# Kernel optimization log

Measured on AMD Instinct MI355X. Metric: run time of the kernel, lower is better.

Reference implementation:

```python
import jax, jax.numpy as jnp
import numpy as np
from jax import lax

LATENT = 512
HIDDEN = 512
VOCAB = 10
SEQ = 6
BATCH = 32768


def setup_inputs() -> dict:
    key = jax.random.key(0)
    ks = jax.random.split(key, 7)
    s_ih = 1.0 / np.sqrt(HIDDEN)
    return {
        "x": jax.random.normal(ks[0], (BATCH, LATENT), dtype=jnp.float32),
        # PyTorch GRU params, gate order (r, z, n)
        "w_ih": jax.random.uniform(ks[1], (3 * HIDDEN, LATENT), jnp.float32, -s_ih, s_ih),
        "w_hh": jax.random.uniform(ks[2], (3 * HIDDEN, HIDDEN), jnp.float32, -s_ih, s_ih),
        "b_ih": jax.random.uniform(ks[3], (3 * HIDDEN,), jnp.float32, -s_ih, s_ih),
        "b_hh": jax.random.uniform(ks[4], (3 * HIDDEN,), jnp.float32, -s_ih, s_ih),
        "w_out": jax.random.uniform(ks[5], (VOCAB, HIDDEN), jnp.float32, -s_ih, s_ih),
        "b_out": jax.random.uniform(ks[6], (VOCAB,), jnp.float32, -s_ih, s_ih),
    }


def reference(x, w_ih, w_hh, b_ih, b_hh, w_out, b_out):
    # Input to the GRU is x repeated at every timestep, so the input-hidden
    # projection is hoisted out of the time loop (computed once).
    gi = x @ w_ih.T + b_ih                      # (B, 3H), constant over time
    gi_r, gi_z, gi_n = jnp.split(gi, 3, axis=-1)

    def step(h, _):
        gh = h @ w_hh.T + b_hh                  # (B, 3H)
        gh_r, gh_z, gh_n = jnp.split(gh, 3, axis=-1)
        r = jax.nn.sigmoid(gi_r + gh_r)
        z = jax.nn.sigmoid(gi_z + gh_z)
        n = jnp.tanh(gi_n + r * gh_n)
        h_new = (1.0 - z) * n + z * h
        return h_new, h_new

    # Initial hidden state is x itself (hidden_dim == latent_dim).
    _, hs = lax.scan(step, x, None, length=SEQ)  # (SEQ, B, H)
    out = jnp.transpose(hs, (1, 0, 2))           # (B, SEQ, H)
    logits = out @ w_out.T + b_out               # (B, SEQ, VOCAB)
    return logits
```

## Files before the change

kernel.cpp:

```cpp
#include <hip/hip_runtime.h>
#include <hip/hip_bf16.h>
#include <stdint.h>


typedef __bf16 bf16_t;
typedef bf16_t bf16x8 __attribute__((ext_vector_type(8)));
typedef bf16_t bf16x4 __attribute__((ext_vector_type(4)));
typedef float  f32x4  __attribute__((ext_vector_type(4)));
typedef float  f32x2  __attribute__((ext_vector_type(2)));

#define THREADS 512
#define BM      64
#define NBLK    512
#define NSTEP   6

#define WIH_OFF 0u
#define WHH_OFF 1572864u
#define WOP_OFF 3145728u
#define GI_OFF  4194304u
#define HST_OFF 104857600u

static __device__ __forceinline__ float sigm(float v) { return 1.0f / (1.0f + __expf(-v)); }
static __device__ __forceinline__ float tanhf_(float v) {
  v = fminf(fmaxf(v, -12.0f), 12.0f);
  float e = __expf(2.0f * v);
  return 1.0f - 2.0f / (e + 1.0f);
}
static __device__ __forceinline__ f32x4 up4(bf16x4 v) {
  f32x4 o; o[0] = (float)v[0]; o[1] = (float)v[1]; o[2] = (float)v[2]; o[3] = (float)v[3];
  return o;
}
static __device__ __forceinline__ bf16x4 pk4(f32x4 v) {
  bf16x4 o; o[0] = (bf16_t)v[0]; o[1] = (bf16_t)v[1]; o[2] = (bf16_t)v[2]; o[3] = (bf16_t)v[3];
  return o;
}

__global__ void prep_kernel(const float* __restrict__ wih_f, const float* __restrict__ whh_f,
                            const float* __restrict__ wout_f,
                            bf16x8* __restrict__ wihPk, bf16x8* __restrict__ whhPk,
                            bf16x8* __restrict__ wopPk) {
  int c = blockIdx.x * 256 + threadIdx.x;
  int lane = c & 63, l15 = lane & 15, lk = (lane >> 4) & 3;
  if (c < 196608) {
    int cid = (c < 98304) ? c : c - 98304;
    const float* src = (c < 98304) ? wih_f : whh_f;
    bf16x8* dst = (c < 98304) ? wihPk : whhPk;
    int kk = (cid >> 6) & 15;
    int nt = cid >> 10;
    const float* p = src + (size_t)(nt * 16 + l15) * 512 + kk * 32 + lk * 8;
    bf16x8 o;
    #pragma unroll
    for (int i = 0; i < 8; ++i) o[i] = (bf16_t)p[i];
    dst[cid] = o;
  } else if (c < 197632) {
    int cid = c - 196608;
    int kk = cid >> 6;
    bf16x8 o;
    if (l15 < 10) {
      const float* p = wout_f + (size_t)l15 * 512 + kk * 32 + lk * 8;
      #pragma unroll
      for (int i = 0; i < 8; ++i) o[i] = (bf16_t)p[i];
    } else {
      #pragma unroll
      for (int i = 0; i < 8; ++i) o[i] = (bf16_t)0.0f;
    }
    wopPk[cid] = o;
  }
}

__global__ __launch_bounds__(THREADS, 2) void gru_kernel(
    const float* __restrict__ x, const float* __restrict__ b_ih,
    const float* __restrict__ b_hh, const float* __restrict__ b_out,
    const bf16x8* __restrict__ wih, const bf16x8* __restrict__ whh,
    const bf16x8* __restrict__ wop,
    bf16x4* __restrict__ gi, bf16x4* __restrict__ hst, float* __restrict__ out) {
  __shared__ __align__(16) char hlds[BM * 1024];

  const int tid   = (int)threadIdx.x;
  const int lane  = tid & 63;
  const int wq    = tid >> 6;
  const int l15   = lane & 15;
  const int lk    = lane >> 4;
  const int brow0 = (int)blockIdx.x * BM;
  const int swz   = (l15 & 7) << 4;
  const int kbase = (lk * 16) ^ swz;
  const int cbase = (lk * 8) ^ swz;

  #pragma unroll
  for (int it = 0; it < 16; ++it) {
    int f4  = it * THREADS + tid;
    int row = f4 >> 7, c4 = f4 & 127;
    float4 v = ((const float4*)(x + (size_t)(brow0 + row) * 512))[c4];
    bf16x4 h4 = { (bf16_t)v.x, (bf16_t)v.y, (bf16_t)v.z, (bf16_t)v.w };
    *(bf16x4*)(&hlds[row * 1024 + ((c4 * 8) ^ ((row & 7) << 4))]) = h4;
  }
  __syncthreads();

  const size_t gibase = (size_t)blockIdx.x * 24576;
  const size_t hstbase = (size_t)blockIdx.x * 8192;

  #pragma unroll
  for (int p = 0; p < 4; ++p) {
    const int jt = wq * 4 + p;
    f32x4 acc[3][4];
    #pragma unroll
    for (int g = 0; g < 3; ++g)
      #pragma unroll
      for (int bt = 0; bt < 4; ++bt) acc[g][bt] = (f32x4){0.f, 0.f, 0.f, 0.f};

    #pragma unroll 2
    for (int kk = 0; kk < 16; ++kk) {
      bf16x8 hf[4];
      #pragma unroll
      for (int bt = 0; bt < 4; ++bt)
        hf[bt] = *(const bf16x8*)(&hlds[(bt * 16 + l15) * 1024 + ((kk * 64) ^ kbase)]);
      #pragma unroll
      for (int g = 0; g < 3; ++g) {
        bf16x8 wf = wih[((g * 32 + jt) * 16 + kk) * 64 + lane];
        #pragma unroll
        for (int bt = 0; bt < 4; ++bt)
          acc[g][bt] = __builtin_amdgcn_mfma_f32_16x16x32_bf16(wf, hf[bt], acc[g][bt], 0, 0, 0);
      }
    }
    {
      int j = jt * 16 + lk * 4;
      f32x4 b0 = *(const f32x4*)(b_ih + j) + *(const f32x4*)(b_hh + j);
      f32x4 b1 = *(const f32x4*)(b_ih + 512 + j) + *(const f32x4*)(b_hh + 512 + j);
      f32x4 b2 = *(const f32x4*)(b_ih + 1024 + j);
      #pragma unroll
      for (int bt = 0; bt < 4; ++bt) {
        int cb = (jt * 3) * 4 + bt;
        gi[gibase + ((size_t)(cb + 0) << 6) + lane] = pk4(acc[0][bt] + b0);
        gi[gibase + ((size_t)(cb + 4) << 6) + lane] = pk4(acc[1][bt] + b1);
        gi[gibase + ((size_t)(cb + 8) << 6) + lane] = pk4(acc[2][bt] + b2);
      }
    }
  }

  for (int t = 0; t < NSTEP; ++t) {
    #pragma unroll
    for (int p = 0; p < 4; ++p) {
      const int jt = wq * 4 + p;
      const int cb = (jt * 3) * 4;

      f32x4 acc[3][4];
      #pragma unroll
      for (int g = 0; g < 3; ++g)
        #pragma unroll
        for (int bt = 0; bt < 4; ++bt) acc[g][bt] = (f32x4){0.f, 0.f, 0.f, 0.f};

      #pragma unroll 2
      for (int kk = 0; kk < 16; ++kk) {
        bf16x8 hf[4];
        #pragma unroll
        for (int bt = 0; bt < 4; ++bt)
          hf[bt] = *(const bf16x8*)(&hlds[(bt * 16 + l15) * 1024 + ((kk * 64) ^ kbase)]);
        #pragma unroll
        for (int g = 0; g < 3; ++g) {
          bf16x8 wf = whh[((g * 32 + jt) * 16 + kk) * 64 + lane];
          #pragma unroll
          for (int bt = 0; bt < 4; ++bt)
            acc[g][bt] = __builtin_amdgcn_mfma_f32_16x16x32_bf16(wf, hf[bt], acc[g][bt], 0, 0, 0);
        }
      }
      {
        int j = jt * 16 + lk * 4;
        f32x4 bn4 = *(const f32x4*)(b_hh + 1024 + j);
        #pragma unroll
        for (int bt = 0; bt < 4; ++bt) {
          bf16x4 grp = gi[gibase + ((size_t)(cb + 0 + bt) << 6) + lane];
          bf16x4 gzp = gi[gibase + ((size_t)(cb + 4 + bt) << 6) + lane];
          bf16x4 gnp = gi[gibase + ((size_t)(cb + 8 + bt) << 6) + lane];
          bf16x4 ho  = *(const bf16x4*)(&hlds[(bt * 16 + l15) * 1024 +
                                              ((jt * 32) ^ cbase)]);
          f32x4 gr = up4(grp), gz = up4(gzp), gn = up4(gnp), hov = up4(ho);
          f32x4 hv;
          #pragma unroll
          for (int r = 0; r < 4; ++r) {
            float rv = sigm(gr[r] + acc[0][bt][r]);
            float zv = sigm(gz[r] + acc[1][bt][r]);
            float nv = tanhf_(gn[r] + rv * (acc[2][bt][r] + bn4[r]));
            hv[r] = (1.0f - zv) * nv + zv * hov[r];
          }
          hst[hstbase + ((size_t)((jt << 2) + bt) << 6) + lane] = pk4(hv);
        }
      }
    }
    __syncthreads();

    #pragma unroll
    for (int p = 0; p < 4; ++p) {
      const int jt = wq * 4 + p;
      #pragma unroll
      for (int bt = 0; bt < 4; ++bt) {
        bf16x4 v = hst[hstbase + ((size_t)((jt << 2) + bt) << 6) + lane];
        *(bf16x4*)(&hlds[(bt * 16 + l15) * 1024 + ((jt * 32) ^ cbase)]) = v;
      }
    }
    __syncthreads();

    if (wq < 4) {
      f32x4 lacc = (f32x4){0.f, 0.f, 0.f, 0.f};
      #pragma unroll 2
      for (int kk = 0; kk < 16; ++kk) {
        bf16x8 hf = *(const bf16x8*)(&hlds[(wq * 16 + l15) * 1024 + ((kk * 64) ^ kbase)]);
        bf16x8 wf = wop[kk * 64 + lane];
        lacc = __builtin_amdgcn_mfma_f32_16x16x32_bf16(wf, hf, lacc, 0, 0, 0);
      }
      size_t ob = (size_t)(brow0 + wq * 16 + l15) * 60 + t * 10 + lk * 4;
      if (lk < 2) {
        f32x2 a = { lacc[0] + b_out[lk * 4 + 0], lacc[1] + b_out[lk * 4 + 1] };
        f32x2 b = { lacc[2] + b_out[lk * 4 + 2], lacc[3] + b_out[lk * 4 + 3] };
        *(f32x2*)(out + ob) = a;
        *(f32x2*)(out + ob + 2) = b;
      } else if (lk == 2) {
        f32x2 a = { lacc[0] + b_out[8], lacc[1] + b_out[9] };
        *(f32x2*)(out + ob) = a;
      }
    }
  }
}

extern "C" void kernel_launch(void* const* d_in, const int* in_sizes, int n_in,
                              void* d_out, int out_size, void* d_ws, size_t ws_size,
                              hipStream_t stream) {
  const float* x     = (const float*)d_in[0];
  const float* wih_f = (const float*)d_in[1];
  const float* whh_f = (const float*)d_in[2];
  const float* b_ih  = (const float*)d_in[3];
  const float* b_hh  = (const float*)d_in[4];
  const float* wout  = (const float*)d_in[5];
  const float* b_out = (const float*)d_in[6];

  char* ws = (char*)d_ws;
  bf16x8* wihPk = (bf16x8*)(ws + WIH_OFF);
  bf16x8* whhPk = (bf16x8*)(ws + WHH_OFF);
  bf16x8* wopPk = (bf16x8*)(ws + WOP_OFF);
  bf16x4* gi    = (bf16x4*)(ws + GI_OFF);
  bf16x4* hst   = (bf16x4*)(ws + HST_OFF);

  prep_kernel<<<772, 256, 0, stream>>>(wih_f, whh_f, wout, wihPk, whhPk, wopPk);
  gru_kernel<<<NBLK, THREADS, 0, stream>>>(x, b_ih, b_hh, b_out,
                                           wihPk, whhPk, wopPk, gi, hst, (float*)d_out);
}
```

Baseline: 600.4 us.

## Switch GRU matmuls to 32x32x16 MFMA tiles with repacked weights

Replaces the 16x16x32 bf16 MFMA tiling with 32x32x16 MFMAs, repacking the weights in the prep kernel to match the new fragment layout. Each wave now owns two 32-wide hidden tiles and two 32-row batch tiles, which cuts LDS fragment reads and weight loads per FLOP. The gate epilogue, hidden-state writeback and output projection are remapped to the 32x32 accumulator layout. Launch bounds drop from 2 to 1 block per CU, allowing more registers for the larger accumulators at the cost of occupancy.

```diff
diff --git a/kernel.cpp b/kernel.cpp
--- a/kernel.cpp
+++ b/kernel.cpp
@@ -7,7 +7,7 @@
 typedef bf16_t bf16x8 __attribute__((ext_vector_type(8)));
 typedef bf16_t bf16x4 __attribute__((ext_vector_type(4)));
 typedef float  f32x4  __attribute__((ext_vector_type(4)));
-typedef float  f32x2  __attribute__((ext_vector_type(2)));
+typedef float  f32x16 __attribute__((ext_vector_type(16)));
 
 #define THREADS 512
 #define BM      64
@@ -40,35 +40,35 @@
                             bf16x8* __restrict__ wihPk, bf16x8* __restrict__ whhPk,
                             bf16x8* __restrict__ wopPk) {
   int c = blockIdx.x * 256 + threadIdx.x;
-  int lane = c & 63, l15 = lane & 15, lk = (lane >> 4) & 3;
+  int lane = c & 63, l31 = lane & 31, hi = (lane >> 5) & 1;
   if (c < 196608) {
     int cid = (c < 98304) ? c : c - 98304;
     const float* src = (c < 98304) ? wih_f : whh_f;
     bf16x8* dst = (c < 98304) ? wihPk : whhPk;
-    int kk = (cid >> 6) & 15;
-    int nt = cid >> 10;
-    const float* p = src + (size_t)(nt * 16 + l15) * 512 + kk * 32 + lk * 8;
+    int chunk = cid >> 6;
+    int kk = chunk & 31;
+    int nt = chunk >> 5;
+    const float* p = src + (size_t)(nt * 32 + l31) * 512 + kk * 16 + hi * 8;
     bf16x8 o;
     #pragma unroll
     for (int i = 0; i < 8; ++i) o[i] = (bf16_t)p[i];
-    dst[cid] = o;
-  } else if (c < 197632) {
-    int cid = c - 196608;
-    int kk = cid >> 6;
+    dst[chunk * 64 + lane] = o;
+  } else if (c < 198656) {
+    int chunk = (c - 196608) >> 6;
     bf16x8 o;
-    if (l15 < 10) {
-      const float* p = wout_f + (size_t)l15 * 512 + kk * 32 + lk * 8;
+    if (l31 < 10) {
+      const float* p = wout_f + (size_t)l31 * 512 + chunk * 16 + hi * 8;
       #pragma unroll
       for (int i = 0; i < 8; ++i) o[i] = (bf16_t)p[i];
     } else {
       #pragma unroll
       for (int i = 0; i < 8; ++i) o[i] = (bf16_t)0.0f;
     }
-    wopPk[cid] = o;
-  }
-}
-
-__global__ __launch_bounds__(THREADS, 2) void gru_kernel(
+    wopPk[chunk * 64 + lane] = o;
+  }
+}
+
+__global__ __launch_bounds__(THREADS, 1) void gru_kernel(
     const float* __restrict__ x, const float* __restrict__ b_ih,
     const float* __restrict__ b_hh, const float* __restrict__ b_out,
     const bf16x8* __restrict__ wih, const bf16x8* __restrict__ whh,
@@ -79,12 +79,11 @@
   const int tid   = (int)threadIdx.x;
   const int lane  = tid & 63;
   const int wq    = tid >> 6;
-  const int l15   = lane & 15;
-  const int lk    = lane >> 4;
+  const int l31   = lane & 31;
+  const int hi    = lane >> 5;
   const int brow0 = (int)blockIdx.x * BM;
-  const int swz   = (l15 & 7) << 4;
-  const int kbase = (lk * 16) ^ swz;
-  const int cbase = (lk * 8) ^ swz;
+  const int rswz  = (l31 & 7) << 4;
+  const int kcol  = hi * 16;
 
   #pragma unroll
   for (int it = 0; it < 16; ++it) {
@@ -100,122 +99,131 @@
   const size_t hstbase = (size_t)blockIdx.x * 8192;
 
   #pragma unroll
-  for (int p = 0; p < 4; ++p) {
-    const int jt = wq * 4 + p;
-    f32x4 acc[3][4];
-    #pragma unroll
-    for (int g = 0; g < 3; ++g)
-      #pragma unroll
-      for (int bt = 0; bt < 4; ++bt) acc[g][bt] = (f32x4){0.f, 0.f, 0.f, 0.f};
-
+  for (int p = 0; p < 2; ++p) {
+    const int jt = wq * 2 + p;
+    f32x16 aR[2], aZ[2], aN[2];
+    #pragma unroll
+    for (int bt = 0; bt < 2; ++bt) {
+      aR[bt] = (f32x16)(0.0f); aZ[bt] = (f32x16)(0.0f); aN[bt] = (f32x16)(0.0f);
+    }
     #pragma unroll 2
-    for (int kk = 0; kk < 16; ++kk) {
-      bf16x8 hf[4];
-      #pragma unroll
-      for (int bt = 0; bt < 4; ++bt)
-        hf[bt] = *(const bf16x8*)(&hlds[(bt * 16 + l15) * 1024 + ((kk * 64) ^ kbase)]);
-      #pragma unroll
-      for (int g = 0; g < 3; ++g) {
-        bf16x8 wf = wih[((g * 32 + jt) * 16 + kk) * 64 + lane];
+    for (int kk = 0; kk < 32; ++kk) {
+      bf16x8 wfR = wih[((0 * 512) + jt * 32 + kk) * 64 + lane];
+      bf16x8 wfZ = wih[((1 * 512) + jt * 32 + kk) * 64 + lane];
+      bf16x8 wfN = wih[((2 * 512) + jt * 32 + kk) * 64 + lane];
+      bf16x8 hf0 = *(const bf16x8*)(&hlds[(0 * 32 + l31) * 1024 + ((kk * 32 + kcol) ^ rswz)]);
+      bf16x8 hf1 = *(const bf16x8*)(&hlds[(1 * 32 + l31) * 1024 + ((kk * 32 + kcol) ^ rswz)]);
+      aR[0] = __builtin_amdgcn_mfma_f32_32x32x16_bf16(wfR, hf0, aR[0], 0, 0, 0);
+      aR[1] = __builtin_amdgcn_mfma_f32_32x32x16_bf16(wfR, hf1, aR[1], 0, 0, 0);
+      aZ[0] = __builtin_amdgcn_mfma_f32_32x32x16_bf16(wfZ, hf0, aZ[0], 0, 0, 0);
+      aZ[1] = __builtin_amdgcn_mfma_f32_32x32x16_bf16(wfZ, hf1, aZ[1], 0, 0, 0);
+      aN[0] = __builtin_amdgcn_mfma_f32_32x32x16_bf16(wfN, hf0, aN[0], 0, 0, 0);
+      aN[1] = __builtin_amdgcn_mfma_f32_32x32x16_bf16(wfN, hf1, aN[1], 0, 0, 0);
+    }
+    #pragma unroll
+    for (int bt = 0; bt < 2; ++bt)
+      #pragma unroll
+      for (int grp = 0; grp < 4; ++grp) {
+        int j0 = jt * 32 + grp * 8 + hi * 4;
+        f32x4 bR = *(const f32x4*)(b_ih + j0) + *(const f32x4*)(b_hh + j0);
+        f32x4 bZ = *(const f32x4*)(b_ih + 512 + j0) + *(const f32x4*)(b_hh + 512 + j0);
+        f32x4 bN = *(const f32x4*)(b_ih + 1024 + j0);
+        f32x4 vR, vZ, vN;
         #pragma unroll
-        for (int bt = 0; bt < 4; ++bt)
-          acc[g][bt] = __builtin_amdgcn_mfma_f32_16x16x32_bf16(wf, hf[bt], acc[g][bt], 0, 0, 0);
-      }
-    }
-    {
-      int j = jt * 16 + lk * 4;
-      f32x4 b0 = *(const f32x4*)(b_ih + j) + *(const f32x4*)(b_hh + j);
-      f32x4 b1 = *(const f32x4*)(b_ih + 512 + j) + *(const f32x4*)(b_hh + 512 + j);
-      f32x4 b2 = *(const f32x4*)(b_ih + 1024 + j);
-      #pragma unroll
-      for (int bt = 0; bt < 4; ++bt) {
-        int cb = (jt * 3) * 4 + bt;
-        gi[gibase + ((size_t)(cb + 0) << 6) + lane] = pk4(acc[0][bt] + b0);
-        gi[gibase + ((size_t)(cb + 4) << 6) + lane] = pk4(acc[1][bt] + b1);
-        gi[gibase + ((size_t)(cb + 8) << 6) + lane] = pk4(acc[2][bt] + b2);
-      }
-    }
+        for (int i = 0; i < 4; ++i) {
+          vR[i] = aR[bt][grp * 4 + i] + bR[i];
+          vZ[i] = aZ[bt][grp * 4 + i] + bZ[i];
+          vN[i] = aN[bt][grp * 4 + i] + bN[i];
+        }
+        int cb = ((jt * 3) * 2 + bt) * 4 + grp;
+        gi[gibase + ((size_t)(cb + 0) << 6) + lane] = pk4(vR);
+        gi[gibase + ((size_t)(cb + 8) << 6) + lane] = pk4(vZ);
+        gi[gibase + ((size_t)(cb + 16) << 6) + lane] = pk4(vN);
+      }
   }
 
   for (int t = 0; t < NSTEP; ++t) {
     #pragma unroll
-    for (int p = 0; p < 4; ++p) {
-      const int jt = wq * 4 + p;
-      const int cb = (jt * 3) * 4;
-
-      f32x4 acc[3][4];
-      #pragma unroll
-      for (int g = 0; g < 3; ++g)
+    for (int p = 0; p < 2; ++p) {
+      const int jt = wq * 2 + p;
+      f32x16 aR[2], aZ[2], aN[2];
+      #pragma unroll
+      for (int bt = 0; bt < 2; ++bt) {
+        aR[bt] = (f32x16)(0.0f); aZ[bt] = (f32x16)(0.0f); aN[bt] = (f32x16)(0.0f);
+      }
+      #pragma unroll 2
+      for (int kk = 0; kk < 32; ++kk) {
+        bf16x8 wfR = whh[((0 * 512) + jt * 32 + kk) * 64 + lane];
+        bf16x8 wfZ = whh[((1 * 512) + jt * 32 + kk) * 64 + lane];
+        bf16x8 wfN = whh[((2 * 512) + jt * 32 + kk) * 64 + lane];
+        bf16x8 hf0 = *(const bf16x8*)(&hlds[(0 * 32 + l31) * 1024 + ((kk * 32 + kcol) ^ rswz)]);
+        bf16x8 hf1 = *(const bf16x8*)(&hlds[(1 * 32 + l31) * 1024 + ((kk * 32 + kcol) ^ rswz)]);
+        aR[0] = __builtin_amdgcn_mfma_f32_32x32x16_bf16(wfR, hf0, aR[0], 0, 0, 0);
+        aR[1] = __builtin_amdgcn_mfma_f32_32x32x16_bf16(wfR, hf1, aR[1], 0, 0, 0);
+        aZ[0] = __builtin_amdgcn_mfma_f32_32x32x16_bf16(wfZ, hf0, aZ[0], 0, 0, 0);
+        aZ[1] = __builtin_amdgcn_mfma_f32_32x32x16_bf16(wfZ, hf1, aZ[1], 0, 0, 0);
+        aN[0] = __builtin_amdgcn_mfma_f32_32x32x16_bf16(wfN, hf0, aN[0], 0, 0, 0);
+        aN[1] = __builtin_amdgcn_mfma_f32_32x32x16_bf16(wfN, hf1, aN[1], 0, 0, 0);
+      }
+      #pragma unroll
+      for (int bt = 0; bt < 2; ++bt)
         #pragma unroll
-        for (int bt = 0; bt < 4; ++bt) acc[g][bt] = (f32x4){0.f, 0.f, 0.f, 0.f};
-
-      #pragma unroll 2
-      for (int kk = 0; kk < 16; ++kk) {
-        bf16x8 hf[4];
-        #pragma unroll
-        for (int bt = 0; bt < 4; ++bt)
-          hf[bt] = *(const bf16x8*)(&hlds[(bt * 16 + l15) * 1024 + ((kk * 64) ^ kbase)]);
-        #pragma unroll
-        for (int g = 0; g < 3; ++g) {
-          bf16x8 wf = whh[((g * 32 + jt) * 16 + kk) * 64 + lane];
-          #pragma unroll
-          for (int bt = 0; bt < 4; ++bt)
-            acc[g][bt] = __builtin_amdgcn_mfma_f32_16x16x32_bf16(wf, hf[bt], acc[g][bt], 0, 0, 0);
-        }
-      }
-      {
-        int j = jt * 16 + lk * 4;
-        f32x4 bn4 = *(const f32x4*)(b_hh + 1024 + j);
-        #pragma unroll
-        for (int bt = 0; bt < 4; ++bt) {
-          bf16x4 grp = gi[gibase + ((size_t)(cb + 0 + bt) << 6) + lane];
-          bf16x4 gzp = gi[gibase + ((size_t)(cb + 4 + bt) << 6) + lane];
-          bf16x4 gnp = gi[gibase + ((size_t)(cb + 8 + bt) << 6) + lane];
-          bf16x4 ho  = *(const bf16x4*)(&hlds[(bt * 16 + l15) * 1024 +
-                                              ((jt * 32) ^ cbase)]);
-          f32x4 gr = up4(grp), gz = up4(gzp), gn = up4(gnp), hov = up4(ho);
+        for (int grp = 0; grp < 4; ++grp) {
+          int cb = ((jt * 3) * 2 + bt) * 4 + grp;
+          int j0 = jt * 32 + grp * 8 + hi * 4;
+          f32x4 gr  = up4(gi[gibase + ((size_t)(cb + 0) << 6) + lane]);
+          f32x4 gz  = up4(gi[gibase + ((size_t)(cb + 8) << 6) + lane]);
+          f32x4 gn  = up4(gi[gibase + ((size_t)(cb + 16) << 6) + lane]);
+          f32x4 bn4 = *(const f32x4*)(b_hh + 1024 + j0);
+          f32x4 hov = up4(*(const bf16x4*)(&hlds[(bt * 32 + l31) * 1024 +
+                                                 ((jt * 64 + grp * 16 + hi * 8) ^ rswz)]));
           f32x4 hv;
           #pragma unroll
-          for (int r = 0; r < 4; ++r) {
-            float rv = sigm(gr[r] + acc[0][bt][r]);
-            float zv = sigm(gz[r] + acc[1][bt][r]);
-            float nv = tanhf_(gn[r] + rv * (acc[2][bt][r] + bn4[r]));
-            hv[r] = (1.0f - zv) * nv + zv * hov[r];
+          for (int i = 0; i < 4; ++i) {
+            int q = grp * 4 + i;
+            float rv = sigm(gr[i] + aR[bt][q]);
+            float zv = sigm(gz[i] + aZ[bt][q]);
+            float nv = tanhf_(gn[i] + rv * (aN[bt][q] + bn4[i]));
+            hv[i] = (1.0f - zv) * nv + zv * hov[i];
           }
-          hst[hstbase + ((size_t)((jt << 2) + bt) << 6) + lane] = pk4(hv);
+          hst[hstbase + ((size_t)((jt * 2 + bt) * 4 + grp) << 6) + lane] = pk4(hv);
         }
-      }
     }
     __syncthreads();
 
     #pragma unroll
-    for (int p = 0; p < 4; ++p) {
-      const int jt = wq * 4 + p;
-      #pragma unroll
-      for (int bt = 0; bt < 4; ++bt) {
-        bf16x4 v = hst[hstbase + ((size_t)((jt << 2) + bt) << 6) + lane];
-        *(bf16x4*)(&hlds[(bt * 16 + l15) * 1024 + ((jt * 32) ^ cbase)]) = v;
-      }
+    for (int p = 0; p < 2; ++p) {
+      const int jt = wq * 2 + p;
+      #pragma unroll
+      for (int bt = 0; bt < 2; ++bt)
+        #pragma unroll
+        for (int grp = 0; grp < 4; ++grp) {
+          bf16x4 v = hst[hstbase + ((size_t)((jt * 2 + bt) * 4 + grp) << 6) + lane];
+          *(bf16x4*)(&hlds[(bt * 32 + l31) * 1024 +
+                           ((jt * 64 + grp * 16 + hi * 8) ^ rswz)]) = v;
+        }
     }
     __syncthreads();
 
-    if (wq < 4) {
-      f32x4 lacc = (f32x4){0.f, 0.f, 0.f, 0.f};
+    if (wq < 2) {
+      f32x16 lacc = (f32x16)(0.0f);
       #pragma unroll 2
-      for (int kk = 0; kk < 16; ++kk) {
-        bf16x8 hf = *(const bf16x8*)(&hlds[(wq * 16 + l15) * 1024 + ((kk * 64) ^ kbase)]);
+      for (int kk = 0; kk < 32; ++kk) {
+        bf16x8 hf = *(const bf16x8*)(&hlds[(wq * 32 + l31) * 1024 + ((kk * 32 + kcol) ^ rswz)]);
         bf16x8 wf = wop[kk * 64 + lane];
-        lacc = __builtin_amdgcn_mfma_f32_16x16x32_bf16(wf, hf, lacc, 0, 0, 0);
-      }
-      size_t ob = (size_t)(brow0 + wq * 16 + l15) * 60 + t * 10 + lk * 4;
-      if (lk < 2) {
-        f32x2 a = { lacc[0] + b_out[lk * 4 + 0], lacc[1] + b_out[lk * 4 + 1] };
-        f32x2 b = { lacc[2] + b_out[lk * 4 + 2], lacc[3] + b_out[lk * 4 + 3] };
-        *(f32x2*)(out + ob) = a;
-        *(f32x2*)(out + ob + 2) = b;
-      } else if (lk == 2) {
-        f32x2 a = { lacc[0] + b_out[8], lacc[1] + b_out[9] };
-        *(f32x2*)(out + ob) = a;
+        lacc = __builtin_amdgcn_mfma_f32_32x32x16_bf16(wf, hf, lacc, 0, 0, 0);
+      }
+      size_t base = (size_t)(brow0 + wq * 32 + l31) * 60 + t * 10;
+      if (hi == 0) {
+        f32x4 v0 = { lacc[0] + b_out[0], lacc[1] + b_out[1],
+                     lacc[2] + b_out[2], lacc[3] + b_out[3] };
+        *(f32x4*)(out + base) = v0;
+        out[base + 8] = lacc[4] + b_out[8];
+        out[base + 9] = lacc[5] + b_out[9];
+      } else {
+        f32x4 v1 = { lacc[0] + b_out[4], lacc[1] + b_out[5],
+                     lacc[2] + b_out[6], lacc[3] + b_out[7] };
+        *(f32x4*)(out + base + 4) = v1;
       }
     }
   }
@@ -239,7 +247,7 @@
   bf16x4* gi    = (bf16x4*)(ws + GI_OFF);
   bf16x4* hst   = (bf16x4*)(ws + HST_OFF);
 
-  prep_kernel<<<772, 256, 0, stream>>>(wih_f, whh_f, wout, wihPk, whhPk, wopPk);
+  prep_kernel<<<776, 256, 0, stream>>>(wih_f, whh_f, wout, wihPk, whhPk, wopPk);
   gru_kernel<<<NBLK, THREADS, 0, stream>>>(x, b_ih, b_hh, b_out,
                                            wihPk, whhPk, wopPk, gi, hst, (float*)d_out);
 }
```

Result: slower. 1.082 ms (+80.2%).
